# Optimization experiments

Hardware: AMD Instinct MI355X
Metric: run time of the kernel (lower is better)

Reference implementation:

```python
import jax, jax.numpy as jnp
import numpy as np

WIDTH = 1024
NUM_HEADS = 16
HEAD_DIM = WIDTH // NUM_HEADS  # 64
WINDOW = 256
BATCH = 2
SEQ = 2048
_MIN_LOGITS_VALUE = -1e30


def setup_inputs() -> dict:
    key = jax.random.key(0)
    ks = jax.random.split(key, 6)
    std = 1.0 / np.sqrt(WIDTH)
    x = jax.random.normal(ks[0], (BATCH, SEQ, WIDTH), dtype=jnp.float32)
    Wq = jax.random.normal(ks[1], (WIDTH, WIDTH), dtype=jnp.float32) * std
    Wk = jax.random.normal(ks[2], (HEAD_DIM, WIDTH), dtype=jnp.float32) * std
    Wv = jax.random.normal(ks[3], (HEAD_DIM, WIDTH), dtype=jnp.float32) * std
    Wf = jax.random.normal(ks[4], (WIDTH, WIDTH), dtype=jnp.float32) * std  # variance_scale=1.0
    bf = jnp.zeros((WIDTH,), dtype=jnp.float32)
    return {"x": x, "Wq": Wq, "Wk": Wk, "Wv": Wv, "Wf": Wf, "bf": bf}


def reference(x, Wq, Wk, Wv, Wf, bf):
    b, t, _ = x.shape
    # projections (torch Linear: y = x @ W.T)
    q = (x @ Wq.T).reshape(b, t, NUM_HEADS, HEAD_DIM)  # b t n h
    k = x @ Wk.T  # b t h  (MQA: single shared key head)
    v = x @ Wv.T  # b t h
    scale = 1.0 / np.sqrt(HEAD_DIM)
    # logits: queries per-head against the shared key head
    logits = jnp.einsum('btnh,bsh->bnts', q, k) * scale  # b n t s
    # symmetric local window mask |i - j| <= WINDOW
    pos = jnp.arange(t)
    mask = jnp.abs(pos[:, None] - pos[None, :]) <= WINDOW  # t s
    masked = jnp.where(mask[None, None, :, :], logits, _MIN_LOGITS_VALUE)
    probs = jax.nn.softmax(masked.astype(jnp.float32), axis=-1).astype(logits.dtype)
    out = jnp.einsum('bnts,bsh->btnh', probs, v).reshape(b, t, WIDTH)
    return out @ Wf.T + bf
```

## Files before the change

kernel.cpp:

```cpp
#include <hip/hip_runtime.h>

typedef __bf16 bf16;
typedef __bf16 bf16x8 __attribute__((ext_vector_type(8)));
typedef float  f32x4  __attribute__((ext_vector_type(4)));

#define MFMA(a, b, c) __builtin_amdgcn_mfma_f32_16x16x32_bf16((a), (b), (c), 0, 0, 0)

static constexpr int B_   = 2;
static constexpr int T_   = 2048;
static constexpr int D_   = 1024;
static constexpr int NH_  = 16;
static constexpr int HD_  = 64;
static constexpr int WIN_ = 256;
static constexpr int M_   = B_ * T_;
static constexpr int NQKV = D_ + 2 * HD_;

__device__ __forceinline__ void gld_lds16(const bf16* g, bf16* l) {
  __builtin_amdgcn_global_load_lds(
      (const __attribute__((address_space(1))) void*)g,
      (__attribute__((address_space(3))) void*)l, 16, 0, 0);
}

__global__ __launch_bounds__(256) void conv_all(
    const float* __restrict__ x,  const float* __restrict__ wq,
    const float* __restrict__ wk, const float* __restrict__ wv,
    const float* __restrict__ wf, const float* __restrict__ bv,
    bf16* __restrict__ xc, bf16* __restrict__ wqkv,
    bf16* __restrict__ wfc, bf16* __restrict__ bfc) {
  const long i = (long)(blockIdx.x * 256 + threadIdx.x) * 4;
  const float* src; bf16* dst; long off;
  if      (i < 4194304L) { src = x;  dst = xc;              off = 0; }
  else if (i < 5242880L) { src = wq; dst = wqkv;            off = 4194304L; }
  else if (i < 5308416L) { src = wk; dst = wqkv + 1048576L; off = 5242880L; }
  else if (i < 5373952L) { src = wv; dst = wqkv + 1114112L; off = 5308416L; }
  else if (i < 6422528L) { src = wf; dst = wfc;             off = 5373952L; }
  else if (i < 6423552L) { src = bv; dst = bfc;             off = 6422528L; }
  else return;
  const long j = i - off;
  const float4 v = *(const float4*)(src + j);
  bf16 o[4] = {(bf16)v.x, (bf16)v.y, (bf16)v.z, (bf16)v.w};
  *(uint2*)(dst + j) = *(const uint2*)o;
}

template <int EPI>
__global__ __launch_bounds__(256) void gemm64x128(
    const bf16* __restrict__ A, const bf16* __restrict__ Bw,
    void* __restrict__ Cout, const bf16* __restrict__ bias,
    bf16* __restrict__ kb, bf16* __restrict__ vT, int N, int K) {
  __shared__ __align__(16) bf16 As[64 * 64];
  __shared__ __align__(16) bf16 Bs[128 * 64];

  const int tid  = threadIdx.x;
  const int w    = tid >> 6;
  const int lane = tid & 63;
  const int quad = lane >> 4;
  const int l16  = lane & 15;
  const int wm   = w & 1;
  const int wn   = w >> 1;
  const int m0   = blockIdx.x * 64;
  const int n0   = blockIdx.y * 128;
  const int lrow = lane >> 3;
  const int lcol = (lane & 7) * 8;

  f32x4 acc[2][4] = {};

  for (int k0 = 0; k0 < K; k0 += 64) {
    __syncthreads();
#pragma unroll
    for (int t = 0; t < 6; ++t) {
      const int inst = w * 6 + t;
      if (inst < 8) {
        gld_lds16(&A[(size_t)(m0 + inst * 8 + lrow) * K + k0 + lcol],
                  &As[inst * 512]);
      } else {
        const int bi = inst - 8;
        gld_lds16(&Bw[(size_t)(n0 + bi * 8 + lrow) * K + k0 + lcol],
                  &Bs[bi * 512]);
      }
    }
    __syncthreads();
#pragma unroll
    for (int kk = 0; kk < 64; kk += 32) {
      bf16x8 a[2], b[4];
#pragma unroll
      for (int i = 0; i < 2; ++i)
        a[i] = *(const bf16x8*)&As[(wm * 32 + i * 16 + l16) * 64 + kk + quad * 8];
#pragma unroll
      for (int j = 0; j < 4; ++j)
        b[j] = *(const bf16x8*)&Bs[(wn * 64 + j * 16 + l16) * 64 + kk + quad * 8];
#pragma unroll
      for (int i = 0; i < 2; ++i)
#pragma unroll
        for (int j = 0; j < 4; ++j) acc[i][j] = MFMA(a[i], b[j], acc[i][j]);
    }
  }

#pragma unroll
  for (int i = 0; i < 2; ++i) {
#pragma unroll
    for (int j = 0; j < 4; ++j) {
      const int col     = n0 + wn * 64 + j * 16 + l16;
      const int rowbase = m0 + wm * 32 + i * 16 + quad * 4;
      if (EPI == 1) {
        if (col < D_) {
          bf16* qb = (bf16*)Cout;
#pragma unroll
          for (int r = 0; r < 4; ++r)
            qb[(size_t)(rowbase + r) * D_ + col] = (bf16)(acc[i][j][r] * 0.125f);
        } else if (col < D_ + HD_) {
#pragma unroll
          for (int r = 0; r < 4; ++r)
            kb[(size_t)(rowbase + r) * HD_ + (col - D_)] = (bf16)acc[i][j][r];
        } else {
          bf16 o[4] = {(bf16)acc[i][j][0], (bf16)acc[i][j][1],
                       (bf16)acc[i][j][2], (bf16)acc[i][j][3]};
          *(uint2*)&vT[(size_t)(col - D_ - HD_) * M_ + rowbase] = *(const uint2*)o;
        }
      } else {
        float* outp = (float*)Cout;
        const float bvv = (float)bias[col];
#pragma unroll
        for (int r = 0; r < 4; ++r)
          outp[(size_t)(rowbase + r) * D_ + col] = acc[i][j][r] + bvv;
      }
    }
  }
}

__global__ __launch_bounds__(256) void attn_win128(
    const bf16* __restrict__ q, const bf16* __restrict__ k,
    const bf16* __restrict__ vT, bf16* __restrict__ o) {
  __shared__ __align__(16) bf16 Qs[128 * 64];
  __shared__ __align__(16) bf16 Ks[2][64 * 64];
  __shared__ __align__(16) bf16 Vt[2][64 * 64];
  __shared__ __align__(16) bf16 Ps[128 * 72];
  __shared__ float ls[4][32];

  const int tid  = threadIdx.x;
  const int w    = tid >> 6;
  const int lane = tid & 63;
  const int quad = lane >> 4;
  const int l16  = lane & 15;
  const int lrow = lane >> 3;
  const int lcol = (lane & 7) * 8;

  const int t0 = blockIdx.x * 128;
  const int n  = blockIdx.y;
  const int b  = blockIdx.z;

#pragma unroll
  for (int t = 0; t < 4; ++t) {
    const int inst = w * 4 + t;
    gld_lds16(&q[((size_t)(b * T_ + t0 + inst * 8 + lrow)) * D_ + n * HD_ + lcol],
              &Qs[inst * 512]);
  }

  auto stageKV = [&](int st, int pb) {
#pragma unroll
    for (int t = 0; t < 2; ++t) {
      const int inst = w * 2 + t;
      gld_lds16(&k[((size_t)(b * T_ + st + inst * 8 + lrow)) * HD_ + lcol],
                &Ks[pb][inst * 512]);
      gld_lds16(&vT[(size_t)(inst * 8 + lrow) * M_ + b * T_ + st + lcol],
                &Vt[pb][inst * 512]);
    }
  };

  const int st_lo = (t0 - WIN_ > 0) ? t0 - WIN_ : 0;
  const int st_hi = (t0 + WIN_ + 64 < T_ - 64) ? t0 + WIN_ + 64 : T_ - 64;

  stageKV(st_lo, 0);
  int pb = 0;

  f32x4 o_acc[2][4] = {};
  float l_part[2] = {0.0f, 0.0f};

  for (int st = st_lo; st <= st_hi; st += 64) {
    __syncthreads();
    if (st + 64 <= st_hi) stageKV(st + 64, pb ^ 1);

    f32x4 sacc[4][2] = {};
#pragma unroll
    for (int kk = 0; kk < 64; kk += 32) {
      bf16x8 ak[4], bq[2];
#pragma unroll
      for (int stile = 0; stile < 4; ++stile)
        ak[stile] = *(const bf16x8*)&Ks[pb][(stile * 16 + l16) * 64 + kk + quad * 8];
#pragma unroll
      for (int tt = 0; tt < 2; ++tt)
        bq[tt] = *(const bf16x8*)&Qs[(w * 32 + tt * 16 + l16) * 64 + kk + quad * 8];
#pragma unroll
      for (int stile = 0; stile < 4; ++stile)
#pragma unroll
        for (int tt = 0; tt < 2; ++tt)
          sacc[stile][tt] = MFMA(ak[stile], bq[tt], sacc[stile][tt]);
    }

    const int off_t = st - t0;
    const bool need_mask =
        (off_t < w * 32 - (WIN_ - 31)) || (off_t > w * 32 + (WIN_ - 63));
    if (!need_mask) {
#pragma unroll
      for (int tt = 0; tt < 2; ++tt) {
#pragma unroll
        for (int stile = 0; stile < 4; ++stile) {
          bf16 pk[4];
          float psum = 0.0f;
#pragma unroll
          for (int r = 0; r < 4; ++r) {
            const float p = __expf(fminf(sacc[stile][tt][r], 30.0f));
            psum += p;
            pk[r] = (bf16)p;
          }
          l_part[tt] += psum;
          *(uint2*)&Ps[(w * 32 + tt * 16 + l16) * 72 + stile * 16 + quad * 4] =
              *(const uint2*)pk;
        }
      }
    } else {
#pragma unroll
      for (int tt = 0; tt < 2; ++tt) {
        const int t = t0 + w * 32 + tt * 16 + l16;
#pragma unroll
        for (int stile = 0; stile < 4; ++stile) {
          bf16 pk[4];
          float psum = 0.0f;
#pragma unroll
          for (int r = 0; r < 4; ++r) {
            const int s = st + stile * 16 + quad * 4 + r;
            const int d = t - s;
            const float p = (d > WIN_ || d < -WIN_)
                                ? 0.0f
                                : __expf(fminf(sacc[stile][tt][r], 30.0f));
            psum += p;
            pk[r] = (bf16)p;
          }
          l_part[tt] += psum;
          *(uint2*)&Ps[(w * 32 + tt * 16 + l16) * 72 + stile * 16 + quad * 4] =
              *(const uint2*)pk;
        }
      }
    }
    __syncthreads();

#pragma unroll
    for (int kk = 0; kk < 64; kk += 32) {
      bf16x8 ap[2];
#pragma unroll
      for (int rg = 0; rg < 2; ++rg)
        ap[rg] = *(const bf16x8*)&Ps[(w * 32 + rg * 16 + l16) * 72 + kk + quad * 8];
#pragma unroll
      for (int nt = 0; nt < 4; ++nt) {
        bf16x8 bv = *(const bf16x8*)&Vt[pb][(nt * 16 + l16) * 64 + kk + quad * 8];
#pragma unroll
        for (int rg = 0; rg < 2; ++rg)
          o_acc[rg][nt] = MFMA(ap[rg], bv, o_acc[rg][nt]);
      }
    }
    pb ^= 1;
  }

#pragma unroll
  for (int tt = 0; tt < 2; ++tt) {
    l_part[tt] += __shfl_xor(l_part[tt], 16);
    l_part[tt] += __shfl_xor(l_part[tt], 32);
    if (quad == 0) ls[w][tt * 16 + l16] = l_part[tt];
  }
  __syncthreads();

#pragma unroll
  for (int rg = 0; rg < 2; ++rg) {
#pragma unroll
    for (int r = 0; r < 4; ++r) {
      const float lr = ls[w][rg * 16 + quad * 4 + r] + 1e-30f;
      const int t = t0 + w * 32 + rg * 16 + quad * 4 + r;
#pragma unroll
      for (int nt = 0; nt < 4; ++nt) {
        const int h = nt * 16 + l16;
        o[((size_t)(b * T_ + t)) * D_ + n * HD_ + h] =
            (bf16)(o_acc[rg][nt][r] / lr);
      }
    }
  }
}

extern "C" void kernel_launch(void* const* d_in, const int* in_sizes, int n_in,
                              void* d_out, int out_size, void* d_ws, size_t ws_size,
                              hipStream_t stream) {
  float* out = (float*)d_out;

  bf16* xc   = (bf16*)d_ws;
  bf16* wqkv = xc   + (size_t)M_ * D_;
  bf16* wfc  = wqkv + (size_t)NQKV * D_;
  bf16* bfc  = wfc  + (size_t)D_ * D_;
  bf16* qb   = bfc  + D_;
  bf16* kb   = qb   + (size_t)M_ * D_;
  bf16* vT   = kb   + (size_t)M_ * HD_;

  dim3 blk(256);
  conv_all<<<dim3((6423552 / 4 + 255) / 256), blk, 0, stream>>>(
      (const float*)d_in[0], (const float*)d_in[1], (const float*)d_in[2],
      (const float*)d_in[3], (const float*)d_in[4], (const float*)d_in[5],
      xc, wqkv, wfc, bfc);

  gemm64x128<1><<<dim3(M_ / 64, NQKV / 128), blk, 0, stream>>>(
      xc, wqkv, (void*)qb, nullptr, kb, vT, NQKV, D_);

  attn_win128<<<dim3(T_ / 128, NH_, B_), blk, 0, stream>>>(qb, kb, vT, qb);

  gemm64x128<2><<<dim3(M_ / 64, D_ / 128), blk, 0, stream>>>(
      qb, wfc, (void*)out, bfc, nullptr, nullptr, D_, D_);
}
```

Baseline: 156.2 us.

## Enlarge GEMM tiles to 128x128, keep Q in registers, use exp2 and setprio

Both projection GEMMs now use 128x128 output tiles, giving each wave a 64x64 sub-tile so more MFMA work is done per LDS load. In the attention kernel, Q fragments are read straight from global memory into registers instead of being staged in LDS. The softmax uses exp2 with log2(e) folded into the Q scale, and s_setprio brackets the MFMA bursts. Risks are fewer GEMM blocks (lower occupancy and less wave-level parallelism across CUs) and higher register pressure.

```diff
diff --git a/kernel.cpp b/kernel.cpp
--- a/kernel.cpp
+++ b/kernel.cpp
@@ -14,6 +14,8 @@
 static constexpr int WIN_ = 256;
 static constexpr int M_   = B_ * T_;
 static constexpr int NQKV = D_ + 2 * HD_;
+
+static constexpr float QSCALE = 0.125f * 1.44269504088896f;
 
 __device__ __forceinline__ void gld_lds16(const bf16* g, bf16* l) {
   __builtin_amdgcn_global_load_lds(
@@ -43,11 +45,11 @@
 }
 
 template <int EPI>
-__global__ __launch_bounds__(256) void gemm64x128(
+__global__ __launch_bounds__(256) void gemm128x128(
     const bf16* __restrict__ A, const bf16* __restrict__ Bw,
     void* __restrict__ Cout, const bf16* __restrict__ bias,
     bf16* __restrict__ kb, bf16* __restrict__ vT, int N, int K) {
-  __shared__ __align__(16) bf16 As[64 * 64];
+  __shared__ __align__(16) bf16 As[128 * 64];
   __shared__ __align__(16) bf16 Bs[128 * 64];
 
   const int tid  = threadIdx.x;
@@ -57,23 +59,23 @@
   const int l16  = lane & 15;
   const int wm   = w & 1;
   const int wn   = w >> 1;
-  const int m0   = blockIdx.x * 64;
+  const int m0   = blockIdx.x * 128;
   const int n0   = blockIdx.y * 128;
   const int lrow = lane >> 3;
   const int lcol = (lane & 7) * 8;
 
-  f32x4 acc[2][4] = {};
+  f32x4 acc[4][4] = {};
 
   for (int k0 = 0; k0 < K; k0 += 64) {
     __syncthreads();
 #pragma unroll
-    for (int t = 0; t < 6; ++t) {
-      const int inst = w * 6 + t;
-      if (inst < 8) {
+    for (int t = 0; t < 8; ++t) {
+      const int inst = w * 8 + t;
+      if (inst < 16) {
         gld_lds16(&A[(size_t)(m0 + inst * 8 + lrow) * K + k0 + lcol],
                   &As[inst * 512]);
       } else {
-        const int bi = inst - 8;
+        const int bi = inst - 16;
         gld_lds16(&Bw[(size_t)(n0 + bi * 8 + lrow) * K + k0 + lcol],
                   &Bs[bi * 512]);
       }
@@ -81,32 +83,32 @@
     __syncthreads();
 #pragma unroll
     for (int kk = 0; kk < 64; kk += 32) {
-      bf16x8 a[2], b[4];
-#pragma unroll
-      for (int i = 0; i < 2; ++i)
-        a[i] = *(const bf16x8*)&As[(wm * 32 + i * 16 + l16) * 64 + kk + quad * 8];
+      bf16x8 a[4], b[4];
+#pragma unroll
+      for (int i = 0; i < 4; ++i)
+        a[i] = *(const bf16x8*)&As[(wm * 64 + i * 16 + l16) * 64 + kk + quad * 8];
 #pragma unroll
       for (int j = 0; j < 4; ++j)
         b[j] = *(const bf16x8*)&Bs[(wn * 64 + j * 16 + l16) * 64 + kk + quad * 8];
 #pragma unroll
-      for (int i = 0; i < 2; ++i)
+      for (int i = 0; i < 4; ++i)
 #pragma unroll
         for (int j = 0; j < 4; ++j) acc[i][j] = MFMA(a[i], b[j], acc[i][j]);
     }
   }
 
 #pragma unroll
-  for (int i = 0; i < 2; ++i) {
+  for (int i = 0; i < 4; ++i) {
 #pragma unroll
     for (int j = 0; j < 4; ++j) {
       const int col     = n0 + wn * 64 + j * 16 + l16;
-      const int rowbase = m0 + wm * 32 + i * 16 + quad * 4;
+      const int rowbase = m0 + wm * 64 + i * 16 + quad * 4;
       if (EPI == 1) {
         if (col < D_) {
           bf16* qb = (bf16*)Cout;
 #pragma unroll
           for (int r = 0; r < 4; ++r)
-            qb[(size_t)(rowbase + r) * D_ + col] = (bf16)(acc[i][j][r] * 0.125f);
+            qb[(size_t)(rowbase + r) * D_ + col] = (bf16)(acc[i][j][r] * QSCALE);
         } else if (col < D_ + HD_) {
 #pragma unroll
           for (int r = 0; r < 4; ++r)
@@ -130,7 +132,6 @@
 __global__ __launch_bounds__(256) void attn_win128(
     const bf16* __restrict__ q, const bf16* __restrict__ k,
     const bf16* __restrict__ vT, bf16* __restrict__ o) {
-  __shared__ __align__(16) bf16 Qs[128 * 64];
   __shared__ __align__(16) bf16 Ks[2][64 * 64];
   __shared__ __align__(16) bf16 Vt[2][64 * 64];
   __shared__ __align__(16) bf16 Ps[128 * 72];
@@ -148,13 +149,6 @@
   const int n  = blockIdx.y;
   const int b  = blockIdx.z;
 
-#pragma unroll
-  for (int t = 0; t < 4; ++t) {
-    const int inst = w * 4 + t;
-    gld_lds16(&q[((size_t)(b * T_ + t0 + inst * 8 + lrow)) * D_ + n * HD_ + lcol],
-              &Qs[inst * 512]);
-  }
-
   auto stageKV = [&](int st, int pb) {
 #pragma unroll
     for (int t = 0; t < 2; ++t) {
@@ -172,6 +166,15 @@
   stageKV(st_lo, 0);
   int pb = 0;
 
+  bf16x8 qf[2][2];
+#pragma unroll
+  for (int tt = 0; tt < 2; ++tt)
+#pragma unroll
+    for (int kq = 0; kq < 2; ++kq)
+      qf[tt][kq] = *(const bf16x8*)
+          &q[((size_t)(b * T_ + t0 + w * 32 + tt * 16 + l16)) * D_ +
+             n * HD_ + kq * 32 + quad * 8];
+
   f32x4 o_acc[2][4] = {};
   float l_part[2] = {0.0f, 0.0f};
 
@@ -182,18 +185,17 @@
     f32x4 sacc[4][2] = {};
 #pragma unroll
     for (int kk = 0; kk < 64; kk += 32) {
-      bf16x8 ak[4], bq[2];
+      bf16x8 ak[4];
 #pragma unroll
       for (int stile = 0; stile < 4; ++stile)
         ak[stile] = *(const bf16x8*)&Ks[pb][(stile * 16 + l16) * 64 + kk + quad * 8];
-#pragma unroll
-      for (int tt = 0; tt < 2; ++tt)
-        bq[tt] = *(const bf16x8*)&Qs[(w * 32 + tt * 16 + l16) * 64 + kk + quad * 8];
+      __builtin_amdgcn_s_setprio(1);
 #pragma unroll
       for (int stile = 0; stile < 4; ++stile)
 #pragma unroll
         for (int tt = 0; tt < 2; ++tt)
-          sacc[stile][tt] = MFMA(ak[stile], bq[tt], sacc[stile][tt]);
+          sacc[stile][tt] = MFMA(ak[stile], qf[tt][kk >> 5], sacc[stile][tt]);
+      __builtin_amdgcn_s_setprio(0);
     }
 
     const int off_t = st - t0;
@@ -208,7 +210,8 @@
           float psum = 0.0f;
 #pragma unroll
           for (int r = 0; r < 4; ++r) {
-            const float p = __expf(fminf(sacc[stile][tt][r], 30.0f));
+            const float p =
+                __builtin_amdgcn_exp2f(fminf(sacc[stile][tt][r], 43.28f));
             psum += p;
             pk[r] = (bf16)p;
           }
@@ -229,9 +232,10 @@
           for (int r = 0; r < 4; ++r) {
             const int s = st + stile * 16 + quad * 4 + r;
             const int d = t - s;
-            const float p = (d > WIN_ || d < -WIN_)
-                                ? 0.0f
-                                : __expf(fminf(sacc[stile][tt][r], 30.0f));
+            const float p =
+                (d > WIN_ || d < -WIN_)
+                    ? 0.0f
+                    : __builtin_amdgcn_exp2f(fminf(sacc[stile][tt][r], 43.28f));
             psum += p;
             pk[r] = (bf16)p;
           }
@@ -249,6 +253,7 @@
 #pragma unroll
       for (int rg = 0; rg < 2; ++rg)
         ap[rg] = *(const bf16x8*)&Ps[(w * 32 + rg * 16 + l16) * 72 + kk + quad * 8];
+      __builtin_amdgcn_s_setprio(1);
 #pragma unroll
       for (int nt = 0; nt < 4; ++nt) {
         bf16x8 bv = *(const bf16x8*)&Vt[pb][(nt * 16 + l16) * 64 + kk + quad * 8];
@@ -256,6 +261,7 @@
         for (int rg = 0; rg < 2; ++rg)
           o_acc[rg][nt] = MFMA(ap[rg], bv, o_acc[rg][nt]);
       }
+      __builtin_amdgcn_s_setprio(0);
     }
     pb ^= 1;
   }
@@ -303,11 +309,11 @@
       (const float*)d_in[3], (const float*)d_in[4], (const float*)d_in[5],
       xc, wqkv, wfc, bfc);
 
-  gemm64x128<1><<<dim3(M_ / 64, NQKV / 128), blk, 0, stream>>>(
+  gemm128x128<1><<<dim3(M_ / 128, NQKV / 128), blk, 0, stream>>>(
       xc, wqkv, (void*)qb, nullptr, kb, vT, NQKV, D_);
 
   attn_win128<<<dim3(T_ / 128, NH_, B_), blk, 0, stream>>>(qb, kb, vT, qb);
 
-  gemm64x128<2><<<dim3(M_ / 64, D_ / 128), blk, 0, stream>>>(
+  gemm128x128<2><<<dim3(M_ / 128, D_ / 128), blk, 0, stream>>>(
       qb, wfc, (void*)out, bfc, nullptr, nullptr, D_, D_);
 }
```

Measured after the change: 160.9 us. 1.03x slower.
